# Optimization experiments

Measured on AMD Instinct MI355X. Metric: run time of the kernel, lower is better.

## Reference

```python
import jax, jax.numpy as jnp
import numpy as np

H = 1024      # hidden_size
NH = 16       # n_heads
DK = 64       # d_kv


def setup_inputs() -> dict:
    key = jax.random.key(0)
    k1, k2, k3, k4, k5 = jax.random.split(key, 5)
    x = jax.random.normal(k1, (4, 2048, H), dtype=jnp.float32)
    # dense1: hidden -> 3*n_heads*d_kv
    W1 = jax.random.normal(k2, (H, 3 * NH * DK), dtype=jnp.float32) / np.sqrt(H)
    b1 = jax.random.normal(k3, (3 * NH * DK,), dtype=jnp.float32) * 0.02
    # dense2: n_heads*d_kv -> hidden
    W2 = jax.random.normal(k4, (NH * DK, H), dtype=jnp.float32) / np.sqrt(NH * DK)
    b2 = jax.random.normal(k5, (H,), dtype=jnp.float32) * 0.02
    return {"x": x, "W1": W1, "b1": b1, "W2": W2, "b2": b2}


def reference(x, W1, b1, W2, b2):
    B, S, _ = x.shape
    scale = 1.0 / np.sqrt(DK)
    qkv = x @ W1 + b1                                   # [B,S,3*NH*DK]
    qkv = qkv.reshape(B, S, 3, NH, DK)
    q, k, v = jnp.moveaxis(qkv, 2, 0)                   # each [B,S,NH,DK]
    q = q.transpose(0, 2, 1, 3)                         # [B,NH,S,DK]
    k = k.transpose(0, 2, 1, 3)
    v = v.transpose(0, 2, 1, 3)
    scores = jnp.einsum('bhqd,bhkd->bhqk', q, k) * scale  # [B,NH,S,S]
    attn = jax.nn.softmax(scores, axis=-1)
    ctx = jnp.einsum('bhqk,bhkd->bhqd', attn, v)        # [B,NH,S,DK]
    ctx = ctx.transpose(0, 2, 1, 3).reshape(B, S, NH * DK)
    return ctx @ W2 + b2
```

## Files before the change

### kernel.cpp

```cpp
#include <hip/hip_runtime.h>
#include <hip/hip_bf16.h>


typedef __hip_bfloat16 bf16;
typedef __attribute__((ext_vector_type(8))) short bf16x8;
typedef __attribute__((ext_vector_type(4))) short bf16x4;
typedef __attribute__((ext_vector_type(4))) float f32x4;

#define B_   4
#define S_   2048
#define H_   1024
#define NH_  16
#define DK_  64
#define M_   8192
#define N1_  3072
#define K_   1024

#define SCALE_Q 0.18033688f

typedef const __attribute__((address_space(1))) void* gas_t;
typedef __attribute__((address_space(3))) void* las_t;
#define G2L16(g, l) __builtin_amdgcn_global_load_lds((gas_t)(g), (las_t)(l), 16, 0, 0)

#if __has_builtin(__builtin_amdgcn_exp2f)
#define EX2(x) __builtin_amdgcn_exp2f(x)
#else
#define EX2(x) exp2f(x)
#endif

#if __has_builtin(__builtin_amdgcn_mfma_f32_16x16x16_bf16)
#define MFMA16(a, b, c) __builtin_amdgcn_mfma_f32_16x16x16_bf16(a, b, c, 0, 0, 0)
#else
#define MFMA16(a, b, c) __builtin_amdgcn_mfma_f32_16x16x16bf16_1k(a, b, c, 0, 0, 0)
#endif

__device__ __forceinline__ float b2f(bf16 v) { return __bfloat162float(v); }

__device__ __forceinline__ unsigned pk2(float a, float b) {
    unsigned ua = __float_as_uint(a);
    unsigned ub = __float_as_uint(b);
    ua += 0x7FFFu + ((ua >> 16) & 1u);
    ub += 0x7FFFu + ((ub >> 16) & 1u);
    return (ua >> 16) | (ub & 0xFFFF0000u);
}

__global__ __launch_bounds__(256) void conv_x(const float* __restrict__ X,
                                              bf16* __restrict__ Xb)
{
    size_t i = ((size_t)blockIdx.x * 256 + threadIdx.x) * 8;
    float4 lo = *(const float4*)&X[i];
    float4 hi = *(const float4*)&X[i + 4];
    uint4 u;
    u.x = pk2(lo.x, lo.y); u.y = pk2(lo.z, lo.w);
    u.z = pk2(hi.x, hi.y); u.w = pk2(hi.z, hi.w);
    *(uint4*)&Xb[i] = u;
}

__global__ __launch_bounds__(256) void conv_wT(const float* __restrict__ W,
                                               bf16* __restrict__ WT,
                                               int Kdim, int Ndim)
{
    __shared__ bf16 T[64][72];
    const int tid = threadIdx.x;
    const int n0 = blockIdx.x * 64, k0 = blockIdx.y * 64;
    const int kr = tid >> 4, nc = (tid & 15) * 4;
    #pragma unroll
    for (int p = 0; p < 4; ++p) {
        float4 v = *(const float4*)&W[(size_t)(k0 + kr + p * 16) * Ndim + n0 + nc];
        T[nc + 0][kr + p * 16] = __float2bfloat16(v.x);
        T[nc + 1][kr + p * 16] = __float2bfloat16(v.y);
        T[nc + 2][kr + p * 16] = __float2bfloat16(v.z);
        T[nc + 3][kr + p * 16] = __float2bfloat16(v.w);
    }
    __syncthreads();
    const int nr = tid >> 2, kc = (tid & 3) * 16;
    *(bf16x8*)&WT[(size_t)(n0 + nr) * Kdim + k0 + kc]     = *(const bf16x8*)&T[nr][kc];
    *(bf16x8*)&WT[(size_t)(n0 + nr) * Kdim + k0 + kc + 8] = *(const bf16x8*)&T[nr][kc + 8];
}

__device__ __forceinline__ void qkv_epilogue(
    const f32x4 acc[4][4], const float* __restrict__ B1,
    bf16* __restrict__ Qp, bf16* __restrict__ Kp, bf16* __restrict__ Vt,
    int n0, int m0, int wm, int wn, int quad, int col)
{
    const int which = n0 >> 10;
    const int bb = m0 >> 11;
    if (which == 2) {
        #pragma unroll
        for (int i = 0; i < 4; ++i) {
            int s = (m0 & (S_ - 1)) + wm * 64 + i * 16 + quad * 4;
            #pragma unroll
            for (int j = 0; j < 4; ++j) {
                int n = n0 + wn * 64 + j * 16 + col;
                int h = (n >> 6) & 15, d = n & 63;
                float bv = B1[n];
                uint2 t;
                t.x = pk2(acc[i][j][0] + bv, acc[i][j][1] + bv);
                t.y = pk2(acc[i][j][2] + bv, acc[i][j][3] + bv);
                *(uint2*)&Vt[(((size_t)(bb * NH_ + h)) * DK_ + d) * S_ + s] = t;
            }
        }
    } else {
        bf16* dst = which ? Kp : Qp;
        const float sc = which ? 1.0f : SCALE_Q;
        #pragma unroll
        for (int i = 0; i < 4; ++i) {
            #pragma unroll
            for (int r = 0; r < 4; ++r) {
                int s = (m0 & (S_ - 1)) + wm * 64 + i * 16 + quad * 4 + r;
                #pragma unroll
                for (int j = 0; j < 4; ++j) {
                    int n = n0 + wn * 64 + j * 16 + col;
                    int h = (n >> 6) & 15, d = n & 63;
                    dst[(((size_t)(bb * NH_ + h)) * S_ + s) * DK_ + d] =
                        __float2bfloat16((acc[i][j][r] + B1[n]) * sc);
                }
            }
        }
    }
}

__global__ __launch_bounds__(256) void gemm_qkv_mfma2(
    const bf16* __restrict__ Xb, const bf16* __restrict__ W1T,
    const float* __restrict__ B1,
    bf16* __restrict__ Qp, bf16* __restrict__ Kp, bf16* __restrict__ Vt)
{
    __shared__ bf16 As[128 * 32];
    __shared__ bf16 Bs[128 * 32];

    const int tid = threadIdx.x;
    const int lane = tid & 63, wv = tid >> 6;
    const int col = lane & 15, quad = lane >> 4;
    const int wm = wv >> 1, wn = wv & 1;
    const int n0 = blockIdx.x * 128, m0 = blockIdx.y * 128;

    f32x4 acc[4][4] = {};

    const bf16* Ag = Xb  + (size_t)m0 * K_;
    const bf16* Bg = W1T + (size_t)n0 * K_;

    for (int k0 = 0; k0 < K_; k0 += 32) {
        #pragma unroll
        for (int h = 0; h < 2; ++h) {
            int idx = tid + h * 256;
            int row = idx >> 2, c = (idx & 3) * 8;
            G2L16(Ag + (size_t)row * K_ + k0 + c, As + (size_t)idx * 8);
            G2L16(Bg + (size_t)row * K_ + k0 + c, Bs + (size_t)idx * 8);
        }
        __syncthreads();

        bf16x8 af[4], bfr[4];
        #pragma unroll
        for (int i = 0; i < 4; ++i)
            af[i] = *(const bf16x8*)&As[(wm * 64 + i * 16 + col) * 32 + quad * 8];
        #pragma unroll
        for (int j = 0; j < 4; ++j)
            bfr[j] = *(const bf16x8*)&Bs[(wn * 64 + j * 16 + col) * 32 + quad * 8];

        #pragma unroll
        for (int i = 0; i < 4; ++i)
            #pragma unroll
            for (int j = 0; j < 4; ++j)
                acc[i][j] = __builtin_amdgcn_mfma_f32_16x16x32_bf16(af[i], bfr[j], acc[i][j], 0, 0, 0);
        __syncthreads();
    }
    qkv_epilogue(acc, B1, Qp, Kp, Vt, n0, m0, wm, wn, quad, col);
}

__global__ __launch_bounds__(256) void gemm_qkv_mfma(
    const float* __restrict__ X, const bf16* __restrict__ W1T,
    const float* __restrict__ B1,
    bf16* __restrict__ Qp, bf16* __restrict__ Kp, bf16* __restrict__ Vt)
{
    __shared__ bf16 As[128 * 32];
    __shared__ bf16 Bs[128 * 32];

    const int tid = threadIdx.x;
    const int lane = tid & 63, wv = tid >> 6;
    const int col = lane & 15, quad = lane >> 4;
    const int wm = wv >> 1, wn = wv & 1;
    const int n0 = blockIdx.x * 128, m0 = blockIdx.y * 128;

    f32x4 acc[4][4] = {};

    const float* Ag = X   + (size_t)m0 * K_;
    const bf16*  Bg = W1T + (size_t)n0 * K_;

    for (int k0 = 0; k0 < K_; k0 += 32) {
        #pragma unroll
        for (int h = 0; h < 2; ++h) {
            int idx = tid + h * 256;
            int row = idx >> 2, c = (idx & 3) * 8;
            G2L16(Bg + (size_t)row * K_ + k0 + c, Bs + (size_t)idx * 8);
        }
        #pragma unroll
        for (int h = 0; h < 2; ++h) {
            int idx = tid + h * 256;
            int row = idx >> 2, c = (idx & 3) * 8;
            float4 lo = *(const float4*)&Ag[(size_t)row * K_ + k0 + c];
            float4 hi = *(const float4*)&Ag[(size_t)row * K_ + k0 + c + 4];
            uint4 u;
            u.x = pk2(lo.x, lo.y); u.y = pk2(lo.z, lo.w);
            u.z = pk2(hi.x, hi.y); u.w = pk2(hi.z, hi.w);
            *(uint4*)&As[(size_t)idx * 8] = u;
        }
        __syncthreads();

        bf16x8 af[4], bfr[4];
        #pragma unroll
        for (int i = 0; i < 4; ++i)
            af[i] = *(const bf16x8*)&As[(wm * 64 + i * 16 + col) * 32 + quad * 8];
        #pragma unroll
        for (int j = 0; j < 4; ++j)
            bfr[j] = *(const bf16x8*)&Bs[(wn * 64 + j * 16 + col) * 32 + quad * 8];

        #pragma unroll
        for (int i = 0; i < 4; ++i)
            #pragma unroll
            for (int j = 0; j < 4; ++j)
                acc[i][j] = __builtin_amdgcn_mfma_f32_16x16x32_bf16(af[i], bfr[j], acc[i][j], 0, 0, 0);
        __syncthreads();
    }
    qkv_epilogue(acc, B1, Qp, Kp, Vt, n0, m0, wm, wn, quad, col);
}

__global__ __launch_bounds__(256, 4) void attn_mfma(
    const bf16* __restrict__ Q, const bf16* __restrict__ K,
    const bf16* __restrict__ Vt, bf16* __restrict__ CTX)
{
    __shared__ bf16 Ks[64][72];
    __shared__ bf16 Vs[64][72];

    const int tid  = threadIdx.x;
    const int wv   = tid >> 6;
    const int lane = tid & 63;
    const int col  = lane & 15;
    const int quad = lane >> 4;

    const int lid = blockIdx.x + (blockIdx.y << 4);
    const int vid = (lid & 7) * 128 + (lid >> 3);
    const int bh = vid >> 4;
    const int q0 = (vid & 15) * 128;

    const bf16* Qg  = Q  + (size_t)bh * S_ * DK_;
    const bf16* Kg  = K  + (size_t)bh * S_ * DK_;
    const bf16* Vtg = Vt + (size_t)bh * DK_ * S_;

    const short oneb = (short)0x3F80;
    const bf16x4 ones4 = {oneb, oneb, oneb, oneb};

    bf16x8 qf[2][2];
    #pragma unroll
    for (int qs = 0; qs < 2; ++qs) {
        const int qrow = q0 + wv * 32 + qs * 16 + col;
        qf[qs][0] = *(const bf16x8*)&Qg[(size_t)qrow * DK_ + quad * 8];
        qf[qs][1] = *(const bf16x8*)&Qg[(size_t)qrow * DK_ + 32 + quad * 8];
    }

    f32x4 o[2][4] = {};
    f32x4 l_acc[2] = {};

    const int sr = tid >> 2;
    const int e0 = (tid & 3) * 16;

    bf16x8 kreg0 = *(const bf16x8*)&Kg[(size_t)sr * DK_ + e0];
    bf16x8 kreg1 = *(const bf16x8*)&Kg[(size_t)sr * DK_ + e0 + 8];
    bf16x8 vreg0 = *(const bf16x8*)&Vtg[(size_t)sr * S_ + e0];
    bf16x8 vreg1 = *(const bf16x8*)&Vtg[(size_t)sr * S_ + e0 + 8];

    for (int kt = 0; kt < S_ / 64; ++kt) {
        *(bf16x8*)&Ks[sr][e0]     = kreg0;
        *(bf16x8*)&Ks[sr][e0 + 8] = kreg1;
        *(bf16x8*)&Vs[sr][e0]     = vreg0;
        *(bf16x8*)&Vs[sr][e0 + 8] = vreg1;
        __syncthreads();

        if (kt + 1 < S_ / 64) {
            kreg0 = *(const bf16x8*)&Kg[(size_t)((kt + 1) * 64 + sr) * DK_ + e0];
            kreg1 = *(const bf16x8*)&Kg[(size_t)((kt + 1) * 64 + sr) * DK_ + e0 + 8];
            vreg0 = *(const bf16x8*)&Vtg[(size_t)sr * S_ + (kt + 1) * 64 + e0];
            vreg1 = *(const bf16x8*)&Vtg[(size_t)sr * S_ + (kt + 1) * 64 + e0 + 8];
        }

        #pragma unroll
        for (int cs = 0; cs < 4; ++cs) {
            const bf16* kb = &Ks[cs * 16 + col][0];
            bf16x8 ka0 = *(const bf16x8*)&kb[quad * 8];
            bf16x8 ka1 = *(const bf16x8*)&kb[32 + quad * 8];
            bf16x4 vf[4];
            #pragma unroll
            for (int ds = 0; ds < 4; ++ds)
                vf[ds] = *(const bf16x4*)&Vs[ds * 16 + col][cs * 16 + quad * 4];

            #pragma unroll
            for (int qs = 0; qs < 2; ++qs) {
                f32x4 a = {0.f, 0.f, 0.f, 0.f};
                a = __builtin_amdgcn_mfma_f32_16x16x32_bf16(ka0, qf[qs][0], a, 0, 0, 0);
                a = __builtin_amdgcn_mfma_f32_16x16x32_bf16(ka1, qf[qs][1], a, 0, 0, 0);
                union { uint2 u; bf16x4 h; } cv;
                cv.u.x = pk2(EX2(a[0]), EX2(a[1]));
                cv.u.y = pk2(EX2(a[2]), EX2(a[3]));
                const bf16x4 pb = cv.h;
                l_acc[qs] = MFMA16(ones4, pb, l_acc[qs]);
                #pragma unroll
                for (int ds = 0; ds < 4; ++ds)
                    o[qs][ds] = MFMA16(vf[ds], pb, o[qs][ds]);
            }
        }
        __syncthreads();
    }

    const int b = bh >> 4, h = bh & 15;
    #pragma unroll
    for (int qs = 0; qs < 2; ++qs) {
        const float inv = 1.f / l_acc[qs][0];
        const int srow = q0 + wv * 32 + qs * 16 + col;
        bf16* crow = CTX + ((size_t)(b * S_ + srow)) * H_ + h * DK_;
        #pragma unroll
        for (int ds = 0; ds < 4; ++ds) {
            uint2 t;
            t.x = pk2(o[qs][ds][0] * inv, o[qs][ds][1] * inv);
            t.y = pk2(o[qs][ds][2] * inv, o[qs][ds][3] * inv);
            *(uint2*)&crow[ds * 16 + quad * 4] = t;
        }
    }
}

__global__ __launch_bounds__(256) void gemm_out_mfma(
    const bf16* __restrict__ Cx, const bf16* __restrict__ W2T,
    const float* __restrict__ B2, float* __restrict__ OUT)
{
    __shared__ bf16 As[128 * 32];
    __shared__ bf16 Bs[128 * 32];

    const int tid = threadIdx.x;
    const int lane = tid & 63, wv = tid >> 6;
    const int col = lane & 15, quad = lane >> 4;
    const int wm = wv >> 1, wn = wv & 1;
    const int n0 = blockIdx.x * 128, m0 = blockIdx.y * 128;

    f32x4 acc[4][4] = {};

    const bf16* Ag = Cx  + (size_t)m0 * K_;
    const bf16* Bg = W2T + (size_t)n0 * K_;

    for (int k0 = 0; k0 < K_; k0 += 32) {
        #pragma unroll
        for (int h = 0; h < 2; ++h) {
            int idx = tid + h * 256;
            int row = idx >> 2, c = (idx & 3) * 8;
            G2L16(Ag + (size_t)row * K_ + k0 + c, As + (size_t)idx * 8);
            G2L16(Bg + (size_t)row * K_ + k0 + c, Bs + (size_t)idx * 8);
        }
        __syncthreads();

        bf16x8 af[4], bfr[4];
        #pragma unroll
        for (int i = 0; i < 4; ++i)
            af[i] = *(const bf16x8*)&As[(wm * 64 + i * 16 + col) * 32 + quad * 8];
        #pragma unroll
        for (int j = 0; j < 4; ++j)
            bfr[j] = *(const bf16x8*)&Bs[(wn * 64 + j * 16 + col) * 32 + quad * 8];

        #pragma unroll
        for (int i = 0; i < 4; ++i)
            #pragma unroll
            for (int j = 0; j < 4; ++j)
                acc[i][j] = __builtin_amdgcn_mfma_f32_16x16x32_bf16(af[i], bfr[j], acc[i][j], 0, 0, 0);
        __syncthreads();
    }

    #pragma unroll
    for (int i = 0; i < 4; ++i) {
        #pragma unroll
        for (int r = 0; r < 4; ++r) {
            int m = m0 + wm * 64 + i * 16 + quad * 4 + r;
            #pragma unroll
            for (int j = 0; j < 4; ++j) {
                int n = n0 + wn * 64 + j * 16 + col;
                OUT[(size_t)m * H_ + n] = acc[i][j][r] + B2[n];
            }
        }
    }
}

extern "C" void kernel_launch(void* const* d_in, const int* in_sizes, int n_in,
                              void* d_out, int out_size, void* d_ws, size_t ws_size,
                              hipStream_t stream)
{
    const float* X  = (const float*)d_in[0];
    const float* W1 = (const float*)d_in[1];
    const float* B1 = (const float*)d_in[2];
    const float* W2 = (const float*)d_in[3];
    const float* B2 = (const float*)d_in[4];
    float* OUT = (float*)d_out;

    const size_t QE = (size_t)B_ * NH_ * S_ * DK_;
    bf16* Qw  = (bf16*)d_ws;
    bf16* Kw  = Qw + QE;
    bf16* Vw  = Kw + QE;
    bf16* Rw  = Vw + QE;
    bf16* W1T = Rw;
    bf16* Cw  = Rw;
    bf16* W2T = Qw;
    bf16* Xb  = Rw + QE;

    const bool fast = ws_size >= 5 * QE * sizeof(bf16);

    conv_wT<<<dim3(N1_ / 64, K_ / 64), 256, 0, stream>>>(W1, W1T, K_, N1_);
    if (fast) {
        conv_x<<<dim3((int)(QE / (256 * 8))), 256, 0, stream>>>(X, Xb);
        gemm_qkv_mfma2<<<dim3(N1_ / 128, M_ / 128), 256, 0, stream>>>(Xb, W1T, B1, Qw, Kw, Vw);
    } else {
        gemm_qkv_mfma<<<dim3(N1_ / 128, M_ / 128), 256, 0, stream>>>(X, W1T, B1, Qw, Kw, Vw);
    }
    attn_mfma<<<dim3(S_ / 128, B_ * NH_), 256, 0, stream>>>(Qw, Kw, Vw, Cw);
    conv_wT<<<dim3(H_ / 64, K_ / 64), 256, 0, stream>>>(W2, W2T, K_, H_);
    gemm_out_mfma<<<dim3(H_ / 128, M_ / 128), 256, 0, stream>>>(Cw, W2T, B2, OUT);
}
```

Baseline: 295.6 us.

## Switch attention kernel to 32x32x16 MFMA tiles with swizzled LDS layout

Rewrites the attention inner loop to use 32x32x16 bf16 MFMA instead of 16x16x32/16x16x16 instructions, so each wave handles its 32 query rows as one tile. The softmax probabilities are repacked across lane halves with a cross-lane shuffle so they can feed the PV and row-sum MFMAs directly. K/V shared-memory tiles get an XOR swizzle to reduce bank conflicts on the new access pattern. This trades fewer, larger matrix instructions and fewer LDS reads for extra shuffles and select logic per tile.

```diff
diff --git a/kernel.cpp b/kernel.cpp
--- a/kernel.cpp
+++ b/kernel.cpp
@@ -4,8 +4,8 @@
 
 typedef __hip_bfloat16 bf16;
 typedef __attribute__((ext_vector_type(8))) short bf16x8;
-typedef __attribute__((ext_vector_type(4))) short bf16x4;
 typedef __attribute__((ext_vector_type(4))) float f32x4;
+typedef __attribute__((ext_vector_type(16))) float f32x16;
 
 #define B_   4
 #define S_   2048
@@ -28,12 +28,6 @@
 #define EX2(x) exp2f(x)
 #endif
 
-#if __has_builtin(__builtin_amdgcn_mfma_f32_16x16x16_bf16)
-#define MFMA16(a, b, c) __builtin_amdgcn_mfma_f32_16x16x16_bf16(a, b, c, 0, 0, 0)
-#else
-#define MFMA16(a, b, c) __builtin_amdgcn_mfma_f32_16x16x16bf16_1k(a, b, c, 0, 0, 0)
-#endif
-
 __device__ __forceinline__ float b2f(bf16 v) { return __bfloat162float(v); }
 
 __device__ __forceinline__ unsigned pk2(float a, float b) {
@@ -42,6 +36,10 @@
     ua += 0x7FFFu + ((ua >> 16) & 1u);
     ub += 0x7FFFu + ((ub >> 16) & 1u);
     return (ua >> 16) | (ub & 0xFFFF0000u);
+}
+
+__device__ __forceinline__ int swzi(int row, int d) {
+    return row * 72 + (d ^ (((row >> 3) & 3) << 3));
 }
 
 __global__ __launch_bounds__(256) void conv_x(const float* __restrict__ X,
@@ -228,14 +226,14 @@
     const bf16* __restrict__ Q, const bf16* __restrict__ K,
     const bf16* __restrict__ Vt, bf16* __restrict__ CTX)
 {
-    __shared__ bf16 Ks[64][72];
-    __shared__ bf16 Vs[64][72];
+    __shared__ bf16 Ks[64 * 72];
+    __shared__ bf16 Vs[64 * 72];
 
     const int tid  = threadIdx.x;
     const int wv   = tid >> 6;
     const int lane = tid & 63;
-    const int col  = lane & 15;
-    const int quad = lane >> 4;
+    const int c32  = lane & 31;
+    const int hi   = lane >> 5;
 
     const int lid = blockIdx.x + (blockIdx.y << 4);
     const int vid = (lid & 7) * 128 + (lid >> 3);
@@ -247,18 +245,17 @@
     const bf16* Vtg = Vt + (size_t)bh * DK_ * S_;
 
     const short oneb = (short)0x3F80;
-    const bf16x4 ones4 = {oneb, oneb, oneb, oneb};
-
-    bf16x8 qf[2][2];
+    const bf16x8 ones8 = {oneb, oneb, oneb, oneb, oneb, oneb, oneb, oneb};
+
+    const int qrow = q0 + wv * 32 + c32;
+    bf16x8 qf[4];
     #pragma unroll
-    for (int qs = 0; qs < 2; ++qs) {
-        const int qrow = q0 + wv * 32 + qs * 16 + col;
-        qf[qs][0] = *(const bf16x8*)&Qg[(size_t)qrow * DK_ + quad * 8];
-        qf[qs][1] = *(const bf16x8*)&Qg[(size_t)qrow * DK_ + 32 + quad * 8];
-    }
-
-    f32x4 o[2][4] = {};
-    f32x4 l_acc[2] = {};
+    for (int dc = 0; dc < 4; ++dc)
+        qf[dc] = *(const bf16x8*)&Qg[(size_t)qrow * DK_ + dc * 16 + hi * 8];
+
+    f32x16 o0 = {};
+    f32x16 o1 = {};
+    f32x16 l_acc = {};
 
     const int sr = tid >> 2;
     const int e0 = (tid & 3) * 16;
@@ -269,10 +266,10 @@
     bf16x8 vreg1 = *(const bf16x8*)&Vtg[(size_t)sr * S_ + e0 + 8];
 
     for (int kt = 0; kt < S_ / 64; ++kt) {
-        *(bf16x8*)&Ks[sr][e0]     = kreg0;
-        *(bf16x8*)&Ks[sr][e0 + 8] = kreg1;
-        *(bf16x8*)&Vs[sr][e0]     = vreg0;
-        *(bf16x8*)&Vs[sr][e0 + 8] = vreg1;
+        *(bf16x8*)&Ks[swzi(sr, e0)]     = kreg0;
+        *(bf16x8*)&Ks[swzi(sr, e0 + 8)] = kreg1;
+        *(bf16x8*)&Vs[swzi(sr, e0)]     = vreg0;
+        *(bf16x8*)&Vs[swzi(sr, e0 + 8)] = vreg1;
         __syncthreads();
 
         if (kt + 1 < S_ / 64) {
@@ -283,46 +280,57 @@
         }
 
         #pragma unroll
-        for (int cs = 0; cs < 4; ++cs) {
-            const bf16* kb = &Ks[cs * 16 + col][0];
-            bf16x8 ka0 = *(const bf16x8*)&kb[quad * 8];
-            bf16x8 ka1 = *(const bf16x8*)&kb[32 + quad * 8];
-            bf16x4 vf[4];
-            #pragma unroll
-            for (int ds = 0; ds < 4; ++ds)
-                vf[ds] = *(const bf16x4*)&Vs[ds * 16 + col][cs * 16 + quad * 4];
-
-            #pragma unroll
-            for (int qs = 0; qs < 2; ++qs) {
-                f32x4 a = {0.f, 0.f, 0.f, 0.f};
-                a = __builtin_amdgcn_mfma_f32_16x16x32_bf16(ka0, qf[qs][0], a, 0, 0, 0);
-                a = __builtin_amdgcn_mfma_f32_16x16x32_bf16(ka1, qf[qs][1], a, 0, 0, 0);
-                union { uint2 u; bf16x4 h; } cv;
-                cv.u.x = pk2(EX2(a[0]), EX2(a[1]));
-                cv.u.y = pk2(EX2(a[2]), EX2(a[3]));
-                const bf16x4 pb = cv.h;
-                l_acc[qs] = MFMA16(ones4, pb, l_acc[qs]);
-                #pragma unroll
-                for (int ds = 0; ds < 4; ++ds)
-                    o[qs][ds] = MFMA16(vf[ds], pb, o[qs][ds]);
-            }
-        }
-        __syncthreads();
-    }
+        for (int ks = 0; ks < 2; ++ks) {
+            f32x16 acc = {};
+            #pragma unroll
+            for (int dc = 0; dc < 4; ++dc) {
+                bf16x8 ka = *(const bf16x8*)&Ks[swzi(ks * 32 + c32, dc * 16 + hi * 8)];
+                acc = __builtin_amdgcn_mfma_f32_32x32x16_bf16(ka, qf[dc], acc, 0, 0, 0);
+            }
+            float e[16];
+            #pragma unroll
+            for (int r = 0; r < 16; ++r) e[r] = EX2(acc[r]);
+            unsigned w[4][2];
+            #pragma unroll
+            for (int g = 0; g < 4; ++g) {
+                w[g][0] = pk2(e[4 * g + 0], e[4 * g + 1]);
+                w[g][1] = pk2(e[4 * g + 2], e[4 * g + 3]);
+            }
+            #pragma unroll
+            for (int c = 0; c < 2; ++c) {
+                unsigned z0 = hi ? w[2 * c][0] : w[2 * c + 1][0];
+                unsigned z1 = hi ? w[2 * c][1] : w[2 * c + 1][1];
+                unsigned x0 = (unsigned)__shfl_xor((int)z0, 32, 64);
+                unsigned x1 = (unsigned)__shfl_xor((int)z1, 32, 64);
+                union { unsigned u[4]; bf16x8 v; } pb;
+                pb.u[0] = hi ? x0 : w[2 * c][0];
+                pb.u[1] = hi ? x1 : w[2 * c][1];
+                pb.u[2] = hi ? w[2 * c + 1][0] : x0;
+                pb.u[3] = hi ? w[2 * c + 1][1] : x1;
+                const int gk = ks * 2 + c;
+                bf16x8 va0 = *(const bf16x8*)&Vs[swzi(c32,      gk * 16 + hi * 8)];
+                bf16x8 va1 = *(const bf16x8*)&Vs[swzi(32 + c32, gk * 16 + hi * 8)];
+                l_acc = __builtin_amdgcn_mfma_f32_32x32x16_bf16(ones8, pb.v, l_acc, 0, 0, 0);
+                o0 = __builtin_amdgcn_mfma_f32_32x32x16_bf16(va0, pb.v, o0, 0, 0, 0);
+                o1 = __builtin_amdgcn_mfma_f32_32x32x16_bf16(va1, pb.v, o1, 0, 0, 0);
+            }
+        }
+        __syncthreads();
+    }
+
+    const float inv = 1.f / l_acc[0];
 
     const int b = bh >> 4, h = bh & 15;
+    bf16* crow = CTX + ((size_t)(b * S_ + qrow)) * H_ + h * DK_;
     #pragma unroll
-    for (int qs = 0; qs < 2; ++qs) {
-        const float inv = 1.f / l_acc[qs][0];
-        const int srow = q0 + wv * 32 + qs * 16 + col;
-        bf16* crow = CTX + ((size_t)(b * S_ + srow)) * H_ + h * DK_;
-        #pragma unroll
-        for (int ds = 0; ds < 4; ++ds) {
-            uint2 t;
-            t.x = pk2(o[qs][ds][0] * inv, o[qs][ds][1] * inv);
-            t.y = pk2(o[qs][ds][2] * inv, o[qs][ds][3] * inv);
-            *(uint2*)&crow[ds * 16 + quad * 4] = t;
-        }
+    for (int g = 0; g < 4; ++g) {
+        uint2 t0, t1;
+        t0.x = pk2(o0[4 * g + 0] * inv, o0[4 * g + 1] * inv);
+        t0.y = pk2(o0[4 * g + 2] * inv, o0[4 * g + 3] * inv);
+        *(uint2*)&crow[g * 8 + hi * 4] = t0;
+        t1.x = pk2(o1[4 * g + 0] * inv, o1[4 * g + 1] * inv);
+        t1.y = pk2(o1[4 * g + 2] * inv, o1[4 * g + 3] * inv);
+        *(uint2*)&crow[32 + g * 8 + hi * 4] = t1;
     }
 }
 
```

New measurement: 310.7 us. 1.05x slower.
